# Optimization experiments

Hardware: AMD Instinct MI355X
Metric: run time of the kernel (lower is better)

The kernel has to match this reference:

```python
import jax, jax.numpy as jnp
import numpy as np

H = 768      # hidden_size
NH = 12      # num_attention_heads
HD = H // NH # head_dim = 64
EPS = 1e-5


def setup_inputs() -> dict:
    key = jax.random.key(0)
    ks = jax.random.split(key, 12)
    B, S = 2, 2048
    s = 1.0 / np.sqrt(H)
    return {
        "hidden_states": jax.random.normal(ks[0], (B, S, H), dtype=jnp.float32),
        "attention_mask": jax.random.normal(ks[1], (B, S), dtype=jnp.float32),
        "Wq": jax.random.normal(ks[2], (H, H), dtype=jnp.float32) * s,
        "bq": jnp.zeros((H,), dtype=jnp.float32),
        "Wk": jax.random.normal(ks[3], (H, H), dtype=jnp.float32) * s,
        "bk": jnp.zeros((H,), dtype=jnp.float32),
        "Wv": jax.random.normal(ks[4], (H, H), dtype=jnp.float32) * s,
        "bv": jnp.zeros((H,), dtype=jnp.float32),
        "Wo": jax.random.normal(ks[5], (H, H), dtype=jnp.float32) * s,
        "bo": jnp.zeros((H,), dtype=jnp.float32),
        "ln_gamma": jnp.ones((H,), dtype=jnp.float32),
        "ln_beta": jnp.zeros((H,), dtype=jnp.float32),
    }


def reference(hidden_states, attention_mask, Wq, bq, Wk, bk, Wv, bv, Wo, bo, ln_gamma, ln_beta):
    B, S, E = hidden_states.shape
    # QKV projections -> [B, NH, S, HD]
    def proj(W, b):
        return (hidden_states @ W + b).reshape(B, S, NH, HD).transpose(0, 2, 1, 3)
    q = proj(Wq, bq)
    k = proj(Wk, bk)
    v = proj(Wv, bv)
    # scores [B, NH, S, S]
    att = jnp.einsum('bhqd,bhkd->bhqk', q, k) * (1.0 / np.sqrt(HD))
    # padding pair mask: valid iff mask>=0 at both query and key positions
    valid = (attention_mask >= 0)  # [B, S]
    pair = valid[:, None, :, None] & valid[:, None, None, :]  # [B,1,S,S]
    att = jnp.where(pair, att, -1e9)
    att = jax.nn.softmax(att, axis=-1)
    # dropout p=0 (eval) -> identity
    ctx = jnp.einsum('bhqk,bhkd->bhqd', att, v)  # [B,NH,S,HD]
    ctx = ctx.transpose(0, 2, 1, 3).reshape(B, S, E)
    # output dense + residual + LayerNorm
    h = ctx @ Wo + bo + hidden_states
    mu = jnp.mean(h, axis=-1, keepdims=True)
    var = jnp.mean(jnp.square(h - mu), axis=-1, keepdims=True)
    out = (h - mu) * jax.lax.rsqrt(var + EPS) * ln_gamma + ln_beta
    return out
```

## Files before the change

kernel.cpp:

```cpp
#include <hip/hip_runtime.h>
#include <hip/hip_bf16.h>

#define H_DIM 768
#define NHEAD 12
#define HDIM  64
#define S_LEN 2048
#define B_SZ  2
#define M_TOT (B_SZ * S_LEN)
#define NQKV  (3 * H_DIM)
#define LN_EPS 1e-5f
#define SM_C   0.1803368801f

typedef __attribute__((ext_vector_type(8)))  short bf16x8;
typedef __attribute__((ext_vector_type(4)))  float f32x4;
typedef __attribute__((ext_vector_type(16))) float f32x16;
typedef __attribute__((ext_vector_type(4)))  int   i32x4;
typedef __attribute__((ext_vector_type(2)))  int   i32x2;

static __device__ inline ushort f2bf(float x) {
    __hip_bfloat16 h = __float2bfloat16(x);
    ushort u;
    __builtin_memcpy(&u, &h, 2);
    return u;
}
static __device__ inline float bf2f(ushort u) {
    unsigned int v = ((unsigned int)u) << 16;
    float f;
    __builtin_memcpy(&f, &v, 4);
    return f;
}
static __device__ inline unsigned pack2bf(float lo, float hi) {
    return (unsigned)f2bf(lo) | ((unsigned)f2bf(hi) << 16);
}

#define GLDS16(g, l) __builtin_amdgcn_global_load_lds( \
    (const __attribute__((address_space(1))) void*)(g), \
    (__attribute__((address_space(3))) void*)(l), 16, 0, 0)

__global__ __launch_bounds__(256)
void prep(const float* __restrict__ hs,
          const float* __restrict__ Wq, const float* __restrict__ Wk,
          const float* __restrict__ Wv, const float* __restrict__ Wo,
          const float* __restrict__ bq, const float* __restrict__ bk,
          const float* __restrict__ bv,
          ushort* __restrict__ Xbf, ushort* __restrict__ Wcat,
          ushort* __restrict__ Wot, float* __restrict__ bcat)
{
    __shared__ ushort T[64][65];
    const int bid = blockIdx.x;
    const int t   = threadIdx.x;

    if (bid < 3072) {
        const int i = (bid * 256 + t) * 4;
        f32x4 v = *(const f32x4*)(hs + i);
        ushort4 o;
        o.x = f2bf(v[0]); o.y = f2bf(v[1]); o.z = f2bf(v[2]); o.w = f2bf(v[3]);
        *(ushort4*)(Xbf + i) = o;
    } else if (bid < 3072 + 576) {
        const int bid2 = bid - 3072;
        const int z = bid2 / 144;
        const int rem = bid2 % 144;
        const int n0 = (rem / 12) * 64;
        const int k0 = (rem % 12) * 64;
        const float* W = (z == 0) ? Wq : (z == 1) ? Wk : (z == 2) ? Wv : Wo;
        const int r = t >> 2, c0 = (t & 3) * 16;
        const float* src = W + (size_t)(k0 + r) * H_DIM + n0 + c0;
        #pragma unroll
        for (int j = 0; j < 16; j += 4) {
            f32x4 v = *(const f32x4*)(src + j);
            #pragma unroll
            for (int jj = 0; jj < 4; ++jj) T[r][c0 + j + jj] = f2bf(v[jj]);
        }
        __syncthreads();
        bf16x8 o0, o1;
        #pragma unroll
        for (int j = 0; j < 8; ++j) {
            o0[j] = (short)T[c0 + j][r];
            o1[j] = (short)T[c0 + 8 + j][r];
        }
        ushort* dst = (z < 3)
            ? Wcat + (size_t)(z * 768 + n0 + r) * H_DIM + k0 + c0
            : Wot  + (size_t)(n0 + r) * H_DIM + k0 + c0;
        *(bf16x8*)dst       = o0;
        *(bf16x8*)(dst + 8) = o1;
    } else {
        const int i = (bid - 3648) * 256 + t;
        if (i < NQKV) {
            float v = (i < 768) ? bq[i] : (i < 1536) ? bk[i - 768] : bv[i - 1536];
            bcat[i] = v;
        }
    }
}

template<int OUTMODE>
__global__ __launch_bounds__(256)
void gemm_mfma(const ushort* __restrict__ A, const ushort* __restrict__ Bt,
               const float* __restrict__ bias, const float* __restrict__ resid,
               void* __restrict__ outp, ushort* __restrict__ vtp,
               int M, int N, int K, int nscale, float sfac)
{
    __shared__ ushort As[128 * 32];
    __shared__ ushort Bs[128 * 32];
    const int bn = blockIdx.x * 128;
    const int bm = blockIdx.y * 128;
    const int t  = threadIdx.x;
    const int w  = t >> 6, l = t & 63;
    const int lg = l >> 4, lr = l & 15;
    const int wr = w >> 1, wc = w & 1;

    f32x4 acc[4][4];
    #pragma unroll
    for (int i = 0; i < 4; ++i)
        #pragma unroll
        for (int j = 0; j < 4; ++j) acc[i][j] = (f32x4){0.f, 0.f, 0.f, 0.f};

    for (int k0 = 0; k0 < K; k0 += 32) {
        #pragma unroll
        for (int it = 0; it < 2; ++it) {
            const int g = it * 256 + t;
            const int r = g >> 2, cb = (g & 3) * 8;
            GLDS16(A  + (size_t)(bm + r) * K + k0 + cb, (char*)As + g * 16);
            GLDS16(Bt + (size_t)(bn + r) * K + k0 + cb, (char*)Bs + g * 16);
        }
        __syncthreads();
        bf16x8 af[4], bfr[4];
        #pragma unroll
        for (int m16 = 0; m16 < 4; ++m16)
            af[m16] = *(const bf16x8*)&As[(wr * 64 + m16 * 16 + lr) * 32 + lg * 8];
        #pragma unroll
        for (int n16 = 0; n16 < 4; ++n16)
            bfr[n16] = *(const bf16x8*)&Bs[(wc * 64 + n16 * 16 + lr) * 32 + lg * 8];
        #pragma unroll
        for (int m16 = 0; m16 < 4; ++m16)
            #pragma unroll
            for (int n16 = 0; n16 < 4; ++n16)
                acc[m16][n16] = __builtin_amdgcn_mfma_f32_16x16x32_bf16(
                    af[m16], bfr[n16], acc[m16][n16], 0, 0, 0);
        __syncthreads();
    }

    #pragma unroll
    for (int m16 = 0; m16 < 4; ++m16) {
        #pragma unroll
        for (int n16 = 0; n16 < 4; ++n16) {
            const int col = bn + wc * 64 + n16 * 16 + lr;
            const float bcol = bias[col];
            const int row0 = bm + wr * 64 + m16 * 16 + lg * 4;
            float vv[4];
            #pragma unroll
            for (int r = 0; r < 4; ++r) {
                float v = acc[m16][n16][r] + bcol;
                if (OUTMODE == 1) v += resid[(size_t)(row0 + r) * N + col];
                else if (col < nscale) v *= sfac;
                vv[r] = v;
            }
            if (OUTMODE == 1) {
                #pragma unroll
                for (int r = 0; r < 4; ++r)
                    ((float*)outp)[(size_t)(row0 + r) * N + col] = vv[r];
            } else if (col >= 1536) {
                const int dfull = col - 1536;
                const int hh = dfull >> 6, dd = dfull & 63;
                const int bb = row0 >> 11, ss = row0 & 2047;
                ushort4 pk;
                pk.x = f2bf(vv[0]); pk.y = f2bf(vv[1]);
                pk.z = f2bf(vv[2]); pk.w = f2bf(vv[3]);
                *(ushort4*)(vtp + ((size_t)(bb * NHEAD + hh) * HDIM + dd) * S_LEN + ss) = pk;
            } else {
                #pragma unroll
                for (int r = 0; r < 4; ++r)
                    ((ushort*)outp)[(size_t)(row0 + r) * N + col] = f2bf(vv[r]);
            }
        }
    }
}

#define KT     64
#define ATT_QT 128
#define KVHALF (S_LEN / 2)
#define NTILES (KVHALF / KT)

__global__ __launch_bounds__(256, 3)
void attn_mfma(const ushort* __restrict__ Qbf, const ushort* __restrict__ Kbf,
               const ushort* __restrict__ Vt, const float* __restrict__ mask,
               ushort* __restrict__ Pp, float* __restrict__ lp)
{
    const int qt = blockIdx.x, h = blockIdx.y;
    const int b  = blockIdx.z >> 1, half = blockIdx.z & 1;
    const int t  = threadIdx.x;
    const int w  = t >> 6, l = t & 63;
    const int l31 = l & 31, hi = l >> 5;
    const int q0 = qt * ATT_QT;
    const int kb0 = half * KVHALF;

    __shared__ ushort Ks[3][KT][64];
    __shared__ ushort Vs[2][HDIM][64];
    __shared__ float  kmarg[KVHALF];

    {
        const int i = t * 4;
        f32x4 v = *(const f32x4*)(mask + b * S_LEN + kb0 + i);
        #pragma unroll
        for (int j = 0; j < 4; ++j)
            kmarg[i + j] = (v[j] >= 0.f) ? 0.f : -1e30f;
    }

    const bool qnL = (mask[b * S_LEN + q0 + w * 32 + l31] < 0.f);

    bf16x8 qa[4];
    {
        const ushort* qsrc = Qbf + (size_t)(b * S_LEN + q0 + w * 32 + l31) * NQKV
                           + h * HDIM + 8 * hi;
        #pragma unroll
        for (int k = 0; k < 4; ++k)
            qa[k] = *(const bf16x8*)(qsrc + 16 * k);
    }

    const int srow = w * 16 + (l >> 3);
    const int scol = ((l & 7) ^ (l >> 3)) * 8;
    const ushort* kLane = Kbf + (size_t)(b * S_LEN + kb0 + srow) * NQKV
                        + h * HDIM + scol;
    const ushort* vLane = Vt + ((size_t)(b * NHEAD + h) * HDIM + srow) * S_LEN
                        + kb0 + scol;
    char* ldsK = (char*)Ks + w * 2048 + l * 16;
    char* ldsV = (char*)Vs + w * 2048 + l * 16;

    __syncthreads();

    GLDS16(kLane, ldsK);
    GLDS16(kLane + (size_t)8 * NQKV, ldsK + 1024);
    GLDS16(vLane, ldsV);
    GLDS16(vLane + (size_t)8 * S_LEN, ldsV + 1024);
    GLDS16(kLane + (size_t)KT * NQKV, ldsK + 8192);
    GLDS16(kLane + (size_t)(KT + 8) * NQKV, ldsK + 8192 + 1024);

    float l_part = 0.f;
    f32x16 accO[2];
    #pragma unroll
    for (int dt = 0; dt < 2; ++dt)
        #pragma unroll
        for (int i = 0; i < 16; ++i) accO[dt][i] = 0.f;

    const int swzl = (l31 & 7) << 4;

    for (int tt = 0; tt < NTILES; ++tt) {
        if (tt < NTILES - 1) {
            asm volatile("s_waitcnt vmcnt(2)" ::: "memory");
        } else {
            asm volatile("s_waitcnt vmcnt(0)" ::: "memory");
        }
        __builtin_amdgcn_s_barrier();

        if (tt + 1 < NTILES) {
            const ushort* vsrc = vLane + (size_t)(tt + 1) * KT;
            char* lv = ldsV + ((tt + 1) & 1) * 8192;
            GLDS16(vsrc, lv);
            GLDS16(vsrc + (size_t)8 * S_LEN, lv + 1024);
            if (tt + 2 < NTILES) {
                const ushort* ksrc = kLane + (size_t)(tt + 2) * KT * NQKV;
                char* lk = ldsK + ((tt + 2) % 3) * 8192;
                GLDS16(ksrc, lk);
                GLDS16(ksrc + (size_t)8 * NQKV, lk + 1024);
            }
        }

        const char* Kc = (const char*)Ks + (tt % 3) * 8192;
        const char* Vc = (const char*)Vs + (tt & 1) * 8192;

        #pragma unroll
        for (int kvt = 0; kvt < 2; ++kvt) {
            f32x16 sc;
            __builtin_amdgcn_s_setprio(1);
            {
                const char* abase = Kc + (kvt * 32 + l31) * 128;
                bf16x8 a0 = *(const bf16x8*)(abase + ((16 * hi +  0) ^ swzl));
                bf16x8 a1 = *(const bf16x8*)(abase + ((16 * hi + 32) ^ swzl));
                bf16x8 a2 = *(const bf16x8*)(abase + ((16 * hi + 64) ^ swzl));
                bf16x8 a3 = *(const bf16x8*)(abase + ((16 * hi + 96) ^ swzl));
                f32x16 z;
                #pragma unroll
                for (int i = 0; i < 16; ++i) z[i] = 0.f;
                sc = __builtin_amdgcn_mfma_f32_32x32x16_bf16(a0, qa[0], z, 0, 0, 0);
                sc = __builtin_amdgcn_mfma_f32_32x32x16_bf16(a1, qa[1], sc, 0, 0, 0);
                sc = __builtin_amdgcn_mfma_f32_32x32x16_bf16(a2, qa[2], sc, 0, 0, 0);
                sc = __builtin_amdgcn_mfma_f32_32x32x16_bf16(a3, qa[3], sc, 0, 0, 0);
            }
            __builtin_amdgcn_s_setprio(0);

            float p[16];
            const float* km = &kmarg[tt * 64 + kvt * 32 + 4 * hi];
            #pragma unroll
            for (int q4 = 0; q4 < 4; ++q4) {
                f32x4 kq = *(const f32x4*)(km + 8 * q4);
                #pragma unroll
                for (int r = 0; r < 4; ++r) {
                    float arg = sc[q4 * 4 + r] + kq[r];
                    arg = qnL ? 0.f : arg;
                    const float pv = exp2f(arg);
                    p[q4 * 4 + r] = pv;
                    l_part += pv;
                }
            }

            __builtin_amdgcn_s_setprio(1);
            #pragma unroll
            for (int cc = 0; cc < 2; ++cc) {
                i32x4 pku;
                pku[0] = (int)pack2bf(p[8 * cc + 0], p[8 * cc + 1]);
                pku[1] = (int)pack2bf(p[8 * cc + 2], p[8 * cc + 3]);
                pku[2] = (int)pack2bf(p[8 * cc + 4], p[8 * cc + 5]);
                pku[3] = (int)pack2bf(p[8 * cc + 6], p[8 * cc + 7]);
                bf16x8 pa;
                __builtin_memcpy(&pa, &pku, 16);
                const int c = kvt * 2 + cc;
                #pragma unroll
                for (int dt = 0; dt < 2; ++dt) {
                    const char* vrow = Vc + (32 * dt + l31) * 128;
                    i32x2 v0 = *(const i32x2*)(vrow + ((32 * c + 8 * hi) ^ swzl));
                    i32x2 v1 = *(const i32x2*)(vrow + ((32 * c + 16 + 8 * hi) ^ swzl));
                    i32x4 vv;
                    vv[0] = v0[0]; vv[1] = v0[1]; vv[2] = v1[0]; vv[3] = v1[1];
                    bf16x8 bv;
                    __builtin_memcpy(&bv, &vv, 16);
                    accO[dt] = __builtin_amdgcn_mfma_f32_32x32x16_bf16(
                        pa, bv, accO[dt], 0, 0, 0);
                }
            }
            __builtin_amdgcn_s_setprio(0);
        }
    }

    l_part += __shfl_xor(l_part, 32, 64);

    const size_t MN = (size_t)M_TOT * H_DIM;
    #pragma unroll
    for (int dt = 0; dt < 2; ++dt) {
        #pragma unroll
        for (int reg = 0; reg < 16; ++reg) {
            const int q = (reg & 3) + 8 * (reg >> 2) + 4 * hi;
            const int m = b * S_LEN + q0 + w * 32 + q;
            Pp[(size_t)half * MN + (size_t)m * H_DIM + h * HDIM + 32 * dt + l31]
                = f2bf(accO[dt][reg]);
        }
    }
    if (hi == 0) {
        const int m = b * S_LEN + q0 + w * 32 + l31;
        lp[half * (M_TOT * NHEAD) + m * NHEAD + h] = l_part;
    }
}

__global__ __launch_bounds__(256)
void combine_kernel(const ushort* __restrict__ Pp, const float* __restrict__ lp,
                    ushort* __restrict__ ctx)
{
    const int idx = blockIdx.x * 256 + threadIdx.x;
    const int m  = idx / 96;
    const int c8 = idx % 96;
    const int c  = c8 * 8;
    const int h  = c8 >> 3;
    const size_t MN = (size_t)M_TOT * H_DIM;

    const float lsum = lp[m * NHEAD + h] + lp[M_TOT * NHEAD + m * NHEAD + h];
    const float inv  = 1.0f / lsum;

    bf16x8 a = *(const bf16x8*)(Pp + (size_t)m * H_DIM + c);
    bf16x8 b = *(const bf16x8*)(Pp + MN + (size_t)m * H_DIM + c);
    bf16x8 o;
    #pragma unroll
    for (int j = 0; j < 8; ++j)
        o[j] = (short)f2bf((bf2f((ushort)a[j]) + bf2f((ushort)b[j])) * inv);
    *(bf16x8*)(ctx + (size_t)m * H_DIM + c) = o;
}

__global__ __launch_bounds__(256)
void ln_kernel(const float* __restrict__ Hbuf, const float* __restrict__ gamma,
               const float* __restrict__ beta, float* __restrict__ out)
{
    const int m = blockIdx.x * 4 + (threadIdx.x >> 6);
    const int l = threadIdx.x & 63;
    const float* row = Hbuf + (size_t)m * H_DIM;

    f32x4 x[3];
    #pragma unroll
    for (int k = 0; k < 3; ++k) x[k] = *(const f32x4*)(row + l * 4 + k * 256);

    float s = 0.f;
    #pragma unroll
    for (int k = 0; k < 3; ++k)
        #pragma unroll
        for (int j = 0; j < 4; ++j) s += x[k][j];
    #pragma unroll
    for (int off = 1; off < 64; off <<= 1) s += __shfl_xor(s, off, 64);
    const float mu = s * (1.0f / H_DIM);

    float v = 0.f;
    #pragma unroll
    for (int k = 0; k < 3; ++k)
        #pragma unroll
        for (int j = 0; j < 4; ++j) {
            const float d = x[k][j] - mu;
            v += d * d;
        }
    #pragma unroll
    for (int off = 1; off < 64; off <<= 1) v += __shfl_xor(v, off, 64);
    const float rstd = rsqrtf(v * (1.0f / H_DIM) + LN_EPS);

    #pragma unroll
    for (int k = 0; k < 3; ++k) {
        const int c = l * 4 + k * 256;
        f32x4 gm = *(const f32x4*)(gamma + c);
        f32x4 bt = *(const f32x4*)(beta + c);
        f32x4 o;
        #pragma unroll
        for (int j = 0; j < 4; ++j)
            o[j] = (x[k][j] - mu) * rstd * gm[j] + bt[j];
        *(f32x4*)(out + (size_t)m * H_DIM + c) = o;
    }
}

extern "C" void kernel_launch(void* const* d_in, const int* in_sizes, int n_in,
                              void* d_out, int out_size, void* d_ws, size_t ws_size,
                              hipStream_t stream)
{
    const float* hs   = (const float*)d_in[0];
    const float* mask = (const float*)d_in[1];
    const float* Wq   = (const float*)d_in[2];
    const float* bq   = (const float*)d_in[3];
    const float* Wk   = (const float*)d_in[4];
    const float* bk   = (const float*)d_in[5];
    const float* Wv   = (const float*)d_in[6];
    const float* bv   = (const float*)d_in[7];
    const float* Wo   = (const float*)d_in[8];
    const float* bo   = (const float*)d_in[9];
    const float* g    = (const float*)d_in[10];
    const float* be   = (const float*)d_in[11];
    float* out = (float*)d_out;

    char* base = (char*)d_ws;
    ushort* Xbf    = (ushort*)(base);
    ushort* QKVbf  = (ushort*)(base + 6291456);
    ushort* Wcat   = (ushort*)(base + 25165824);
    ushort* Wot    = (ushort*)(base + 28704768);
    float*  bcat   = (float*) (base + 29884416);
    ushort* Vt     = (ushort*)(base + 29893632);
    ushort* Cbf    = (ushort*)(base + 36185088);
    float*  Hb     = (float*) (base + 42476544);
    float*  lp     = (float*) (base + 25165824);
    ushort* Pp     = (ushort*)(base + 42476544);

    prep<<<3657, 256, 0, stream>>>(hs, Wq, Wk, Wv, Wo, bq, bk, bv,
                                   Xbf, Wcat, Wot, bcat);

    gemm_mfma<0><<<dim3(NQKV / 128, M_TOT / 128), 256, 0, stream>>>(
        Xbf, Wcat, bcat, nullptr, QKVbf, Vt, M_TOT, NQKV, H_DIM, 768, SM_C);

    attn_mfma<<<dim3(S_LEN / ATT_QT, NHEAD, B_SZ * 2), 256, 0, stream>>>(
        QKVbf, QKVbf + 768, Vt, mask, Pp, lp);

    combine_kernel<<<M_TOT * 96 / 256, 256, 0, stream>>>(Pp, lp, Cbf);

    gemm_mfma<1><<<dim3(H_DIM / 128, M_TOT / 128), 256, 0, stream>>>(
        Cbf, Wot, bo, hs, Hb, nullptr, M_TOT, H_DIM, H_DIM, 0, 1.0f);

    ln_kernel<<<M_TOT / 4, 256, 0, stream>>>(Hb, g, be, out);
}
```

Measured before the change: 125.6 us.

## Permute K rows in LDS to allow 16-byte V reads and remap attention grid

K tile rows are loaded into LDS in a permuted order, and the key-mask indexing is changed to match. This lets each lane read its V operand for the P·V MFMA as one 16-byte LDS load instead of two 8-byte loads plus repacking. The 3D grid is also flattened into 768 blocks with an XCD-aware remap, so blocks sharing a head and batch land on the same XCD for better L2 reuse. It depends on the hardcoded 8-XCD round-robin dispatch assumption and on the permuted K/P ordering staying consistent.

```diff
diff --git a/kernel.cpp b/kernel.cpp
--- a/kernel.cpp
+++ b/kernel.cpp
@@ -15,7 +15,6 @@
 typedef __attribute__((ext_vector_type(4)))  float f32x4;
 typedef __attribute__((ext_vector_type(16))) float f32x16;
 typedef __attribute__((ext_vector_type(4)))  int   i32x4;
-typedef __attribute__((ext_vector_type(2)))  int   i32x2;
 
 static __device__ inline ushort f2bf(float x) {
     __hip_bfloat16 h = __float2bfloat16(x);
@@ -185,8 +184,14 @@
                const ushort* __restrict__ Vt, const float* __restrict__ mask,
                ushort* __restrict__ Pp, float* __restrict__ lp)
 {
-    const int qt = blockIdx.x, h = blockIdx.y;
-    const int b  = blockIdx.z >> 1, half = blockIdx.z & 1;
+    const int flat = blockIdx.x;
+    const int wk   = (flat & 7) * 96 + (flat >> 3);
+    const int qt   = wk & 15;
+    const int c_   = wk >> 4;
+    const int h    = c_ % 12;
+    const int bz   = c_ / 12;
+    const int b    = bz >> 1, half = bz & 1;
+
     const int t  = threadIdx.x;
     const int w  = t >> 6, l = t & 63;
     const int l31 = l & 31, hi = l >> 5;
@@ -216,9 +221,11 @@
             qa[k] = *(const bf16x8*)(qsrc + 16 * k);
     }
 
-    const int srow = w * 16 + (l >> 3);
-    const int scol = ((l & 7) ^ (l >> 3)) * 8;
-    const ushort* kLane = Kbf + (size_t)(b * S_LEN + kb0 + srow) * NQKV
+    const int u    = l >> 3;
+    const int scol = ((l & 7) ^ u) * 8;
+    const int srcK = w * 16 + u + ((u & 4) ? 4 : 0);
+    const int srow = w * 16 + u;
+    const ushort* kLane = Kbf + (size_t)(b * S_LEN + kb0 + srcK) * NQKV
                         + h * HDIM + scol;
     const ushort* vLane = Vt + ((size_t)(b * NHEAD + h) * HDIM + srow) * S_LEN
                         + kb0 + scol;
@@ -228,11 +235,11 @@
     __syncthreads();
 
     GLDS16(kLane, ldsK);
-    GLDS16(kLane + (size_t)8 * NQKV, ldsK + 1024);
+    GLDS16(kLane + (size_t)4 * NQKV, ldsK + 1024);
     GLDS16(vLane, ldsV);
     GLDS16(vLane + (size_t)8 * S_LEN, ldsV + 1024);
     GLDS16(kLane + (size_t)KT * NQKV, ldsK + 8192);
-    GLDS16(kLane + (size_t)(KT + 8) * NQKV, ldsK + 8192 + 1024);
+    GLDS16(kLane + (size_t)(KT + 4) * NQKV, ldsK + 8192 + 1024);
 
     float l_part = 0.f;
     f32x16 accO[2];
@@ -260,7 +267,7 @@
                 const ushort* ksrc = kLane + (size_t)(tt + 2) * KT * NQKV;
                 char* lk = ldsK + ((tt + 2) % 3) * 8192;
                 GLDS16(ksrc, lk);
-                GLDS16(ksrc + (size_t)8 * NQKV, lk + 1024);
+                GLDS16(ksrc + (size_t)4 * NQKV, lk + 1024);
             }
         }
 
@@ -288,10 +295,11 @@
             __builtin_amdgcn_s_setprio(0);
 
             float p[16];
-            const float* km = &kmarg[tt * 64 + kvt * 32 + 4 * hi];
+            const float* km = &kmarg[tt * 64 + kvt * 32];
             #pragma unroll
             for (int q4 = 0; q4 < 4; ++q4) {
-                f32x4 kq = *(const f32x4*)(km + 8 * q4);
+                const int kvb = 16 * (q4 >> 1) + 8 * hi + 4 * (q4 & 1);
+                f32x4 kq = *(const f32x4*)(km + kvb);
                 #pragma unroll
                 for (int r = 0; r < 4; ++r) {
                     float arg = sc[q4 * 4 + r] + kq[r];
@@ -315,13 +323,8 @@
                 const int c = kvt * 2 + cc;
                 #pragma unroll
                 for (int dt = 0; dt < 2; ++dt) {
-                    const char* vrow = Vc + (32 * dt + l31) * 128;
-                    i32x2 v0 = *(const i32x2*)(vrow + ((32 * c + 8 * hi) ^ swzl));
-                    i32x2 v1 = *(const i32x2*)(vrow + ((32 * c + 16 + 8 * hi) ^ swzl));
-                    i32x4 vv;
-                    vv[0] = v0[0]; vv[1] = v0[1]; vv[2] = v1[0]; vv[3] = v1[1];
-                    bf16x8 bv;
-                    __builtin_memcpy(&bv, &vv, 16);
+                    bf16x8 bv = *(const bf16x8*)(Vc + (32 * dt + l31) * 128
+                                                 + ((32 * c + 16 * hi) ^ swzl));
                     accO[dt] = __builtin_amdgcn_mfma_f32_32x32x16_bf16(
                         pa, bv, accO[dt], 0, 0, 0);
                 }
@@ -454,7 +457,7 @@
     gemm_mfma<0><<<dim3(NQKV / 128, M_TOT / 128), 256, 0, stream>>>(
         Xbf, Wcat, bcat, nullptr, QKVbf, Vt, M_TOT, NQKV, H_DIM, 768, SM_C);
 
-    attn_mfma<<<dim3(S_LEN / ATT_QT, NHEAD, B_SZ * 2), 256, 0, stream>>>(
+    attn_mfma<<<768, 256, 0, stream>>>(
         QKVbf, QKVbf + 768, Vt, mask, Pp, lp);
 
     combine_kernel<<<M_TOT * 96 / 256, 256, 0, stream>>>(Pp, lp, Cbf);
```

Result: no change. 123.3 us (-1.8%).
